# Performance work log

Hardware: AMD Instinct MI355X
Metric: run time of the kernel (lower is better)

Reference implementation:

```python
import jax, jax.numpy as jnp
import numpy as np

N = 100000      # nodes
E = 300000      # directed edges (avg degree ~3, ogbn-arxiv-like sparsity)
F_IN = 128      # ogbn-arxiv node features
H = 256         # hidden
C = 40          # ogbn-arxiv classes
L = 6           # num_layers
BN_EPS = 1e-5


def setup_inputs() -> dict:
    key = jax.random.key(0)
    ks = jax.random.split(key, 12)
    x = jax.random.normal(ks[0], (N, F_IN), jnp.float32)
    edge_index = jax.random.randint(ks[1], (2, E), 0, N, dtype=jnp.int32)
    s_in = 1.0 / np.sqrt(F_IN)
    s_h = 1.0 / np.sqrt(H)
    return {
        "x": x,
        "edge_index": edge_index,
        "w_in": jax.random.normal(ks[2], (F_IN, H), jnp.float32) * s_in,
        "b_in": jnp.zeros((H,), jnp.float32),
        "conv_w": jax.random.normal(ks[3], (L, H, H), jnp.float32) * s_h,
        "conv_b": jnp.zeros((L, H), jnp.float32),
        "bn_gamma": jnp.ones((L, H), jnp.float32),
        "bn_beta": jnp.zeros((L, H), jnp.float32),
        "out_w": jax.random.normal(ks[4], (H, C), jnp.float32) * s_h,
        "out_b": jnp.zeros((C,), jnp.float32),
        "res_weights": jax.random.normal(ks[5], (L,), jnp.float32),
    }


def _gcn_norm(edge_index, n_nodes):
    # GCNConv default: add self-loops, symmetric normalization D^-1/2 (A+I) D^-1/2
    loops = jnp.arange(n_nodes, dtype=edge_index.dtype)
    src = jnp.concatenate([edge_index[0], loops])
    dst = jnp.concatenate([edge_index[1], loops])
    deg = jax.ops.segment_sum(jnp.ones_like(dst, jnp.float32), dst, num_segments=n_nodes)
    dinv = jax.lax.rsqrt(jnp.maximum(deg, 1.0))
    norm = dinv[src] * dinv[dst]  # [E+N]
    return src, dst, norm


def _batchnorm(h, gamma, beta):
    # BatchNorm1d in training mode: biased batch statistics over nodes
    m = jnp.mean(h, axis=0)
    v = jnp.mean(jnp.square(h - m), axis=0)
    return (h - m) * jax.lax.rsqrt(v + BN_EPS) * gamma + beta


def reference(x, edge_index, w_in, b_in, conv_w, conv_b, bn_gamma, bn_beta, out_w, out_b, res_weights):
    src, dst, norm = _gcn_norm(edge_index, N)
    h = x @ w_in + b_in            # input_fc: [N, H]
    x_input = h
    layer_out = []
    prev = None
    for i in range(L):
        hw = h @ conv_w[i]                                  # linear transform
        msg = hw[src] * norm[:, None]                       # gather + scale
        agg = jax.ops.segment_sum(msg, dst, num_segments=N) + conv_b[i]  # scatter-add
        a = jax.nn.relu(_batchnorm(agg, bn_gamma[i], bn_beta[i]))
        # dropout p=0.5 omitted (eval mode / deterministic reference)
        if i == 0:
            h = a + 0.2 * x_input
        else:
            h = a + 0.2 * x_input + 0.7 * prev
        layer_out.append(h)
        prev = h
    w = jax.nn.softmax(res_weights)                          # [L]
    mix = jnp.einsum('lnh,l->nh', jnp.stack(layer_out), w)   # weighted sum of layer outputs
    logits = mix @ out_w + out_b                             # [N, C]
    return jax.nn.log_softmax(logits, axis=1)
```

## Files before the change

kernel.cpp:

```cpp
#include <hip/hip_runtime.h>
#include <math.h>

#define Nn   100000
#define Ee   300000
#define FIN  128
#define Hdim 256
#define Ncls 40
#define Lnum 6
#define SCAN_B 98
#define KP   264
#define EMAX 1152

typedef __attribute__((ext_vector_type(8))) short bf16x8;
typedef __attribute__((ext_vector_type(4))) float f32x4;

__device__ __forceinline__ float bf2f(unsigned int u16) {
    unsigned int x = u16 << 16;
    return __builtin_bit_cast(float, x);
}
__device__ __forceinline__ unsigned short f2bf(float f) {
    unsigned int x = __builtin_bit_cast(unsigned int, f);
    x = (x + 0x7FFFu + ((x >> 16) & 1u)) >> 16;
    return (unsigned short)x;
}
__device__ __forceinline__ void unpack2(unsigned int u, float& lo, float& hi) {
    lo = __builtin_bit_cast(float, u << 16);
    hi = __builtin_bit_cast(float, u & 0xFFFF0000u);
}
__device__ __forceinline__ unsigned int pack2(float a, float b) {
    return (unsigned int)f2bf(a) | ((unsigned int)f2bf(b) << 16);
}
__device__ __forceinline__ void acc8(float* a, float w, uint4 v) {
    float f0, f1;
    unpack2(v.x, f0, f1); a[0] += w * f0; a[1] += w * f1;
    unpack2(v.y, f0, f1); a[2] += w * f0; a[3] += w * f1;
    unpack2(v.z, f0, f1); a[4] += w * f0; a[5] += w * f1;
    unpack2(v.w, f0, f1); a[6] += w * f0; a[7] += w * f1;
}

__global__ void count_edges(const int* __restrict__ ei, int* __restrict__ cnt) {
    int e = blockIdx.x * blockDim.x + threadIdx.x;
    if (e < Ee) atomicAdd(&cnt[ei[Ee + e]], 1);
}

__global__ void scan_block(const int* __restrict__ cnt, int* __restrict__ iscan,
                           int* __restrict__ btot) {
    __shared__ int buf[1024];
    int t = threadIdx.x;
    int g = blockIdx.x * 1024 + t;
    int v = (g < Nn) ? cnt[g] : 0;
    buf[t] = v; __syncthreads();
    for (int off = 1; off < 1024; off <<= 1) {
        int x = buf[t];
        int a = (t >= off) ? buf[t - off] : 0;
        __syncthreads();
        buf[t] = x + a;
        __syncthreads();
    }
    if (g < Nn) iscan[g] = buf[t];
    if (t == 1023) btot[blockIdx.x] = buf[1023];
}

__global__ void scan_tops(const int* __restrict__ btot, int* __restrict__ bpref) {
    __shared__ int b[128];
    int t = threadIdx.x;
    int v = (t < SCAN_B) ? btot[t] : 0;
    b[t] = v; __syncthreads();
    for (int off = 1; off < 128; off <<= 1) {
        int x = b[t];
        int a = (t >= off) ? b[t - off] : 0;
        __syncthreads();
        b[t] = x + a;
        __syncthreads();
    }
    if (t < SCAN_B) bpref[t] = b[t] - v;
}

__global__ void scan_final(const int* __restrict__ cnt, const int* __restrict__ iscan,
                           const int* __restrict__ bpref, int* __restrict__ offs,
                           float* __restrict__ dinvp) {
    int g = blockIdx.x * 1024 + threadIdx.x;
    if (g < Nn) {
        int c = cnt[g];
        offs[g] = bpref[blockIdx.x] + iscan[g] - c;
        dinvp[g] = rsqrtf((float)(c + 1));
    }
    if (g == 0) offs[Nn] = Ee;
}

__global__ void fill_csr(const int* __restrict__ ei, const int* __restrict__ offs,
                         int* __restrict__ cur, const float* __restrict__ dinvp,
                         int* __restrict__ esrc, float* __restrict__ ew) {
    int e = blockIdx.x * blockDim.x + threadIdx.x;
    if (e >= Ee) return;
    int s = ei[e], d = ei[Ee + e];
    int p = offs[d] + atomicAdd(&cur[d], 1);
    esrc[p] = s;
    ew[p] = dinvp[s];
}

__global__ void prep_weights(const float* __restrict__ conv_w, const float* __restrict__ w_in,
                             const float* __restrict__ out_w,
                             unsigned short* __restrict__ Whi,
                             unsigned short* __restrict__ Fhi,
                             unsigned short* __restrict__ Whd, unsigned short* __restrict__ Wld) {
    int b = blockIdx.x, t = threadIdx.x;
    if (b < 1536) {
        int id = b * 256 + t;
        int l = id >> 16, k = (id >> 8) & 255, n = id & 255;
        Whi[l * 65536 + n * 256 + k] = f2bf(conv_w[id]);
    } else if (b < 1664) {
        int id = (b - 1536) * 256 + t;
        int k = id >> 8, n = id & 255;
        Fhi[n * FIN + k] = f2bf(w_in[id]);
    } else {
        int id = (b - 1664) * 256 + t;
        int c = id >> 8, k = id & 255;
        float w = (c < Ncls) ? out_w[k * Ncls + c] : 0.f;
        unsigned short hi = f2bf(w);
        unsigned short lo = f2bf(w - bf2f(hi));
        Whd[c * 256 + k] = hi;
        Wld[c * 256 + k] = lo;
    }
}

__global__ void cvt_bf16(const float* __restrict__ src, unsigned short* __restrict__ dst, int n8) {
    int i = blockIdx.x * blockDim.x + threadIdx.x;
    if (i >= n8) return;
    float4 a = ((const float4*)src)[i * 2];
    float4 b = ((const float4*)src)[i * 2 + 1];
    uint4 o;
    o.x = pack2(a.x, a.y); o.y = pack2(a.z, a.w);
    o.z = pack2(b.x, b.y); o.w = pack2(b.z, b.w);
    ((uint4*)dst)[i] = o;
}

__global__ void bn_reduce(const float* __restrict__ P, float* __restrict__ bnsum,
                          float* __restrict__ bnsq, int nb) {
    int c = threadIdx.x;
    int per = (nb + gridDim.x - 1) / gridDim.x;
    int r0 = blockIdx.x * per;
    int r1 = r0 + per; if (r1 > nb) r1 = nb;
    float s = 0.f, q = 0.f;
    for (int r = r0; r < r1; ++r) {
        s += P[(size_t)r * 512 + c];
        q += P[(size_t)r * 512 + 256 + c];
    }
    if (r0 < r1) {
        atomicAdd(&bnsum[c], s);
        atomicAdd(&bnsq[c], q);
    }
}

__global__ __launch_bounds__(512) void gemm_mfma(
    const unsigned short* __restrict__ A, unsigned short* __restrict__ C,
    const unsigned short* __restrict__ W,
    const float* __restrict__ bias, int K, int nrows)
{
    __shared__ __align__(16) unsigned short smem[18432];

    const int t    = threadIdx.x;
    const int lane = t & 63, wid = t >> 6;
    const int ln   = lane & 15, quad = lane >> 4;
    const int r64  = (wid >> 2) * 64, c64 = (wid & 3) * 64;
    const int r0   = blockIdx.x * 128;

    unsigned short* At = smem;
    unsigned short* Bt = smem + 5120;

    f32x4 acc[4][4];
#pragma unroll
    for (int i = 0; i < 4; ++i)
#pragma unroll
        for (int j = 0; j < 4; ++j) acc[i][j] = (f32x4){0.f, 0.f, 0.f, 0.f};

    const int arow = t >> 2, akq = t & 3;
    const bool arow_ok = (r0 + arow < nrows);
    const int nk = K >> 5;

    uint4 ga = make_uint4(0u, 0u, 0u, 0u);
    if (arow_ok) ga = *(const uint4*)&A[(size_t)(r0 + arow) * K + akq * 8];
    uint4 gb[2];
#pragma unroll
    for (int q = 0; q < 2; ++q) {
        int idx = t + 512 * q, row = idx >> 2, kq = idx & 3;
        gb[q] = *(const uint4*)&W[(size_t)row * K + kq * 8];
    }

    for (int kt = 0; kt < nk; ++kt) {
        __syncthreads();
        *(uint4*)&At[arow * 40 + akq * 8] = ga;
#pragma unroll
        for (int q = 0; q < 2; ++q) {
            int idx = t + 512 * q, row = idx >> 2, kq = idx & 3;
            *(uint4*)&Bt[row * 40 + kq * 8] = gb[q];
        }
        __syncthreads();
        if (kt + 1 < nk) {
            int k0 = (kt + 1) << 5;
            ga = make_uint4(0u, 0u, 0u, 0u);
            if (arow_ok) ga = *(const uint4*)&A[(size_t)(r0 + arow) * K + k0 + akq * 8];
#pragma unroll
            for (int q = 0; q < 2; ++q) {
                int idx = t + 512 * q, row = idx >> 2, kq = idx & 3;
                gb[q] = *(const uint4*)&W[(size_t)row * K + k0 + kq * 8];
            }
        }
        bf16x8 af[4], bf[4];
#pragma unroll
        for (int rt = 0; rt < 4; ++rt)
            af[rt] = *(const bf16x8*)&At[(r64 + rt * 16 + ln) * 40 + quad * 8];
#pragma unroll
        for (int ct = 0; ct < 4; ++ct)
            bf[ct] = *(const bf16x8*)&Bt[(c64 + ct * 16 + ln) * 40 + quad * 8];
#pragma unroll
        for (int rt = 0; rt < 4; ++rt)
#pragma unroll
            for (int ct = 0; ct < 4; ++ct)
                acc[rt][ct] = __builtin_amdgcn_mfma_f32_16x16x32_bf16(af[rt], bf[ct], acc[rt][ct], 0, 0, 0);
    }
    __syncthreads();

    float bc[4];
#pragma unroll
    for (int ct = 0; ct < 4; ++ct) bc[ct] = bias[c64 + ct * 16 + ln];

    unsigned short* Tt = &smem[wid * 2304];
    const int rr2 = lane & 31, jh = lane >> 5;
#pragma unroll
    for (int h = 0; h < 2; ++h) {
#pragma unroll
        for (int rr = 0; rr < 2; ++rr) {
            int rt = 2 * h + rr;
#pragma unroll
            for (int ct = 0; ct < 4; ++ct)
#pragma unroll
                for (int v = 0; v < 4; ++v)
                    Tt[(rr * 16 + quad * 4 + v) * 72 + ct * 16 + ln] = f2bf(acc[rt][ct][v] + bc[ct]);
        }
        __asm__ volatile("s_waitcnt lgkmcnt(0)" ::: "memory");
        int grow = r0 + r64 + h * 32 + rr2;
        if (grow < nrows) {
#pragma unroll
            for (int j = 0; j < 4; ++j) {
                uint4 v4 = *(const uint4*)&Tt[rr2 * 72 + jh * 32 + j * 8];
                *(uint4*)&C[(size_t)grow * 256 + c64 + jh * 32 + j * 8] = v4;
            }
        }
        __asm__ volatile("s_waitcnt lgkmcnt(0)" ::: "memory");
    }
}

__global__ __launch_bounds__(512, 4) void gemm_agg(
    const unsigned short* __restrict__ Hin,
    unsigned short* __restrict__ C,
    const unsigned short* __restrict__ W,
    const float* __restrict__ bias,
    const int* __restrict__ offs, const int* __restrict__ esrc,
    const float* __restrict__ ew, const float* __restrict__ dinvp,
    float* __restrict__ bnsum, float* __restrict__ bnsq,
    float* __restrict__ Pstats)
{
    __shared__ __align__(16) unsigned short At[128 * KP];
    __shared__ __align__(16) uint2 eL[EMAX];
    __shared__ int oL[132];
    __shared__ float lsum[256], lsq[256];

    const int t    = threadIdx.x;
    const int lane = t & 63, wid = t >> 6;
    const int ln   = lane & 15, quad = lane >> 4;
    const int r64  = (wid >> 2) * 64, c64 = (wid & 3) * 64;
    const int r0   = blockIdx.x * 128;

    if (t < 256) { lsum[t] = 0.f; lsq[t] = 0.f; }

    const int rEnd = (r0 + 128 <= Nn) ? (r0 + 128) : Nn;
    const int E0 = offs[r0];
    const int E1 = offs[rEnd];
    const int nE = E1 - E0;
    const bool staged = (nE <= EMAX);

    if (t < 129) {
        int idx = r0 + t; if (idx > Nn) idx = Nn;
        oL[t] = offs[idx];
    }
    if (staged) {
        for (int j = t; j < nE; j += 512)
            eL[j] = make_uint2((unsigned)esrc[E0 + j],
                               __builtin_bit_cast(unsigned, ew[E0 + j]));
    }
    __syncthreads();

    const int half = lane >> 5, l31 = lane & 31;
    const int base = wid * 16 + half * 8;
#pragma unroll 1
    for (int p = 0; p < 4; ++p) {
        const int rA = base + 2 * p, rB = rA + 1;
        const int nA = r0 + rA, nB = r0 + rB;
        float a[8] = {0.f,0.f,0.f,0.f,0.f,0.f,0.f,0.f};
        float b[8] = {0.f,0.f,0.f,0.f,0.f,0.f,0.f,0.f};
        int eA = oL[rA], eA1 = oL[rA + 1];
        int eB = oL[rB], eB1 = oL[rB + 1];
        float dnA = 0.f, dnB = 0.f;
        if (nA < Nn) {
            dnA = dinvp[nA];
            uint4 u = *(const uint4*)&Hin[(size_t)nA * Hdim + l31 * 8];
            acc8(a, dnA, u);
        }
        if (nB < Nn) {
            dnB = dinvp[nB];
            uint4 u = *(const uint4*)&Hin[(size_t)nB * Hdim + l31 * 8];
            acc8(b, dnB, u);
        }
        if (staged) {
            while (eA < eA1 || eB < eB1) {
                bool dA = eA < eA1, dB = eB < eB1;
                uint4 vA, vB; float wA = 0.f, wB = 0.f;
                if (dA) {
                    uint2 s = eL[eA - E0];
                    wA = __builtin_bit_cast(float, s.y);
                    vA = *(const uint4*)&Hin[(size_t)s.x * Hdim + l31 * 8];
                }
                if (dB) {
                    uint2 s = eL[eB - E0];
                    wB = __builtin_bit_cast(float, s.y);
                    vB = *(const uint4*)&Hin[(size_t)s.x * Hdim + l31 * 8];
                }
                if (dA) { acc8(a, wA, vA); ++eA; }
                if (dB) { acc8(b, wB, vB); ++eB; }
            }
        } else {
            for (int e = eA; e < eA1; ++e) {
                int s = esrc[e]; float w = ew[e];
                uint4 v = *(const uint4*)&Hin[(size_t)s * Hdim + l31 * 8];
                acc8(a, w, v);
            }
            for (int e = eB; e < eB1; ++e) {
                int s = esrc[e]; float w = ew[e];
                uint4 v = *(const uint4*)&Hin[(size_t)s * Hdim + l31 * 8];
                acc8(b, w, v);
            }
        }
#pragma unroll
        for (int k = 0; k < 8; ++k) { a[k] *= dnA; b[k] *= dnB; }
        *(uint4*)&At[rA * KP + l31 * 8] =
            make_uint4(pack2(a[0], a[1]), pack2(a[2], a[3]),
                       pack2(a[4], a[5]), pack2(a[6], a[7]));
        *(uint4*)&At[rB * KP + l31 * 8] =
            make_uint4(pack2(b[0], b[1]), pack2(b[2], b[3]),
                       pack2(b[4], b[5]), pack2(b[6], b[7]));
    }
    __syncthreads();

    f32x4 acc[4][4];
#pragma unroll
    for (int i = 0; i < 4; ++i)
#pragma unroll
        for (int j = 0; j < 4; ++j) acc[i][j] = (f32x4){0.f, 0.f, 0.f, 0.f};

#pragma unroll
    for (int kt = 0; kt < 8; ++kt) {
        bf16x8 af[4], bf[4];
#pragma unroll
        for (int ct = 0; ct < 4; ++ct)
            bf[ct] = *(const bf16x8*)&W[(size_t)(c64 + ct * 16 + ln) * 256 + kt * 32 + quad * 8];
#pragma unroll
        for (int rt = 0; rt < 4; ++rt)
            af[rt] = *(const bf16x8*)&At[(r64 + rt * 16 + ln) * KP + kt * 32 + quad * 8];
#pragma unroll
        for (int rt = 0; rt < 4; ++rt)
#pragma unroll
            for (int ct = 0; ct < 4; ++ct)
                acc[rt][ct] = __builtin_amdgcn_mfma_f32_16x16x32_bf16(af[rt], bf[ct], acc[rt][ct], 0, 0, 0);
    }

    float bc[4];
#pragma unroll
    for (int ct = 0; ct < 4; ++ct) bc[ct] = bias[c64 + ct * 16 + ln];

#pragma unroll
    for (int ct = 0; ct < 4; ++ct) {
        float s = 0.f, qq = 0.f;
#pragma unroll
        for (int rt = 0; rt < 4; ++rt)
#pragma unroll
            for (int v = 0; v < 4; ++v) {
                int row = r0 + r64 + rt * 16 + quad * 4 + v;
                if (row < Nn) {
                    float val = acc[rt][ct][v] + bc[ct];
                    s += val; qq += val * val;
                }
            }
        s  += __shfl_xor(s, 16);  s  += __shfl_xor(s, 32);
        qq += __shfl_xor(qq, 16); qq += __shfl_xor(qq, 32);
        if (quad == 0) { atomicAdd(&lsum[c64 + ct * 16 + ln], s); atomicAdd(&lsq[c64 + ct * 16 + ln], qq); }
    }

    __syncthreads();

#pragma unroll
    for (int rt = 0; rt < 4; ++rt)
#pragma unroll
        for (int ct = 0; ct < 4; ++ct)
#pragma unroll
            for (int v = 0; v < 4; ++v)
                At[(r64 + rt * 16 + quad * 4 + v) * KP + c64 + ct * 16 + ln] =
                    f2bf(acc[rt][ct][v] + bc[ct]);
    __syncthreads();

    const int l31s = t & 31, rhalf = t >> 5;
#pragma unroll
    for (int p = 0; p < 8; ++p) {
        int lrow = p * 16 + rhalf;
        int grow = r0 + lrow;
        if (grow < Nn) {
            uint4 v4 = *(const uint4*)&At[lrow * KP + l31s * 8];
            *(uint4*)&C[(size_t)grow * 256 + l31s * 8] = v4;
        }
    }

    if (t < 256) {
        if (Pstats) {
            Pstats[(size_t)blockIdx.x * 512 + t]       = lsum[t];
            Pstats[(size_t)blockIdx.x * 512 + 256 + t] = lsq[t];
        } else {
            atomicAdd(&bnsum[t], lsum[t]);
            atomicAdd(&bnsq[t], lsq[t]);
        }
    }
}

__global__ void apply_kernel(const unsigned short* __restrict__ T,
                             const unsigned short* __restrict__ X,
                             unsigned short* __restrict__ Hb, unsigned short* __restrict__ M,
                             const float* __restrict__ bnsum, const float* __restrict__ bnsq,
                             const float* __restrict__ gamma, const float* __restrict__ beta,
                             const float* __restrict__ res_w, int layer) {
    __shared__ float sc[256], sh[256];
    int t = threadIdx.x;
    {
        float mean = bnsum[t] * (1.0f / Nn);
        float var  = fmaxf(bnsq[t] * (1.0f / Nn) - mean * mean, 0.f);
        float rstd = rsqrtf(var + 1e-5f);
        float s = gamma[t] * rstd;
        sc[t] = s; sh[t] = beta[t] - mean * s;
    }
    float m0 = res_w[0];
#pragma unroll
    for (int i = 1; i < Lnum; ++i) m0 = fmaxf(m0, res_w[i]);
    float se = 0.f, wl = 0.f;
#pragma unroll
    for (int i = 0; i < Lnum; ++i) {
        float e = __expf(res_w[i] - m0);
        se += e;
        if (i == layer) wl = e;
    }
    float wi = wl / se;
    __syncthreads();

    int idx = blockIdx.x * blockDim.x + t;
    int c8 = idx & 31;
    float scl[8], shl[8];
#pragma unroll
    for (int k = 0; k < 8; ++k) { scl[k] = sc[c8 * 8 + k]; shl[k] = sh[c8 * 8 + k]; }

    uint4 tv = ((const uint4*)T)[idx];
    uint4 xv = ((const uint4*)X)[idx];
    float tf[8], xf[8];
    unpack2(tv.x, tf[0], tf[1]); unpack2(tv.y, tf[2], tf[3]);
    unpack2(tv.z, tf[4], tf[5]); unpack2(tv.w, tf[6], tf[7]);
    unpack2(xv.x, xf[0], xf[1]); unpack2(xv.y, xf[2], xf[3]);
    unpack2(xv.z, xf[4], xf[5]); unpack2(xv.w, xf[6], xf[7]);

    float a[8];
#pragma unroll
    for (int k = 0; k < 8; ++k)
        a[k] = fmaxf(tf[k] * scl[k] + shl[k], 0.f) + 0.2f * xf[k];
    if (layer > 0) {
        uint4 hv = ((const uint4*)Hb)[idx];
        float hf[8];
        unpack2(hv.x, hf[0], hf[1]); unpack2(hv.y, hf[2], hf[3]);
        unpack2(hv.z, hf[4], hf[5]); unpack2(hv.w, hf[6], hf[7]);
#pragma unroll
        for (int k = 0; k < 8; ++k) a[k] += 0.7f * hf[k];
    }
    uint4 ho;
    ho.x = pack2(a[0], a[1]); ho.y = pack2(a[2], a[3]);
    ho.z = pack2(a[4], a[5]); ho.w = pack2(a[6], a[7]);
    ((uint4*)Hb)[idx] = ho;

    float m[8];
    if (layer == 0) {
#pragma unroll
        for (int k = 0; k < 8; ++k) m[k] = wi * a[k];
    } else {
        uint4 mv = ((const uint4*)M)[idx];
        float mf[8];
        unpack2(mv.x, mf[0], mf[1]); unpack2(mv.y, mf[2], mf[3]);
        unpack2(mv.z, mf[4], mf[5]); unpack2(mv.w, mf[6], mf[7]);
#pragma unroll
        for (int k = 0; k < 8; ++k) m[k] = mf[k] + wi * a[k];
    }
    uint4 mo;
    mo.x = pack2(m[0], m[1]); mo.y = pack2(m[2], m[3]);
    mo.z = pack2(m[4], m[5]); mo.w = pack2(m[6], m[7]);
    ((uint4*)M)[idx] = mo;
}

__global__ __launch_bounds__(512) void head_mfma(const unsigned short* __restrict__ M,
                                                 const unsigned short* __restrict__ Whd,
                                                 const unsigned short* __restrict__ Wld,
                                                 const float* __restrict__ out_b,
                                                 float* __restrict__ out, int nrows) {
    __shared__ unsigned short At[128 * 40];
    const int t    = threadIdx.x;
    const int lane = t & 63, wid = t >> 6;
    const int ln   = lane & 15, quad = lane >> 4;
    const int r0   = blockIdx.x * 128;

    f32x4 acc[3];
#pragma unroll
    for (int ct = 0; ct < 3; ++ct) acc[ct] = (f32x4){0.f, 0.f, 0.f, 0.f};

    for (int k0 = 0; k0 < 256; k0 += 32) {
        __syncthreads();
        {
            int row = t >> 2, kq = t & 3;
            uint4 g = make_uint4(0u, 0u, 0u, 0u);
            if (r0 + row < nrows)
                g = *(const uint4*)&M[(size_t)(r0 + row) * 256 + k0 + kq * 8];
            *(uint4*)&At[row * 40 + kq * 8] = g;
        }
        __syncthreads();
        bf16x8 af = *(const bf16x8*)&At[(wid * 16 + ln) * 40 + quad * 8];
#pragma unroll
        for (int ct = 0; ct < 3; ++ct) {
            int c = ct * 16 + ln;
            bf16x8 bh = *(const bf16x8*)&Whd[c * 256 + k0 + quad * 8];
            bf16x8 bl = *(const bf16x8*)&Wld[c * 256 + k0 + quad * 8];
            acc[ct] = __builtin_amdgcn_mfma_f32_16x16x32_bf16(af, bh, acc[ct], 0, 0, 0);
            acc[ct] = __builtin_amdgcn_mfma_f32_16x16x32_bf16(af, bl, acc[ct], 0, 0, 0);
        }
    }

    int   cc[3]; float bias[3];
#pragma unroll
    for (int ct = 0; ct < 3; ++ct) {
        cc[ct] = ct * 16 + ln;
        bias[ct] = (cc[ct] < Ncls) ? out_b[cc[ct]] : 0.f;
    }
#pragma unroll
    for (int v = 0; v < 4; ++v) {
        int row = r0 + wid * 16 + quad * 4 + v;
        float val[3];
#pragma unroll
        for (int ct = 0; ct < 3; ++ct) val[ct] = acc[ct][v] + bias[ct];
        float mx = -1e30f;
#pragma unroll
        for (int ct = 0; ct < 3; ++ct) if (cc[ct] < Ncls) mx = fmaxf(mx, val[ct]);
        mx = fmaxf(mx, __shfl_xor(mx, 1)); mx = fmaxf(mx, __shfl_xor(mx, 2));
        mx = fmaxf(mx, __shfl_xor(mx, 4)); mx = fmaxf(mx, __shfl_xor(mx, 8));
        float s = 0.f;
#pragma unroll
        for (int ct = 0; ct < 3; ++ct) if (cc[ct] < Ncls) s += __expf(val[ct] - mx);
        s += __shfl_xor(s, 1); s += __shfl_xor(s, 2);
        s += __shfl_xor(s, 4); s += __shfl_xor(s, 8);
        float lse = mx + __logf(s);
        if (row < nrows) {
            out[(size_t)row * Ncls + cc[0]] = val[0] - lse;
            out[(size_t)row * Ncls + cc[1]] = val[1] - lse;
            if (ln < 8) out[(size_t)row * Ncls + cc[2]] = val[2] - lse;
        }
    }
}

extern "C" void kernel_launch(void* const* d_in, const int* in_sizes, int n_in,
                              void* d_out, int out_size, void* d_ws, size_t ws_size,
                              hipStream_t stream)
{
    const float* x      = (const float*)d_in[0];
    const int*   ei     = (const int*)d_in[1];
    const float* w_in   = (const float*)d_in[2];
    const float* b_in   = (const float*)d_in[3];
    const float* conv_w = (const float*)d_in[4];
    const float* conv_b = (const float*)d_in[5];
    const float* gamma  = (const float*)d_in[6];
    const float* beta   = (const float*)d_in[7];
    const float* out_w  = (const float*)d_in[8];
    const float* out_b  = (const float*)d_in[9];
    const float* res_w  = (const float*)d_in[10];
    float* out = (float*)d_out;
    char* ws = (char*)d_ws;

    int*   cnt    = (int*)  (ws + 0);
    int*   cursor = (int*)  (ws + 400000);
    int*   offs   = (int*)  (ws + 800000);
    float* dinvp  = (float*)(ws + 1200016);
    int*   esrc   = (int*)  (ws + 1600016);
    float* ew     = (float*)(ws + 2800016);
    int*   iscan  = (int*)  (ws + 4002064);
    int*   btot   = (int*)  (ws + 4402064);
    int*   bpref  = (int*)  (ws + 4402576);
    unsigned short* Whi = (unsigned short*)(ws + 4403088);
    unsigned short* Fhi = (unsigned short*)(ws + 5975952);
    unsigned short* Whd = (unsigned short*)(ws + 6107024);
    unsigned short* Wld = (unsigned short*)(ws + 6131600);
    unsigned short* X   = (unsigned short*)(ws + 6156176);
    unsigned short* Hb  = X  + (size_t)Nn * Hdim;
    unsigned short* T   = Hb + (size_t)Nn * Hdim;
    unsigned short* M   = T  + (size_t)Nn * Hdim;
    unsigned short* xbf = M;

    float* bnA = (float*)(ws + 4002064);

    const int gblocks = (Nn + 127) / 128;

    const size_t P_OFS = 6156176 + 4 * (size_t)Nn * Hdim * sizeof(unsigned short);
    const size_t P_BYTES = (size_t)gblocks * 512 * sizeof(float);
    float* Pst = (ws_size >= P_OFS + P_BYTES) ? (float*)(ws + P_OFS) : nullptr;

    hipMemsetAsync(cnt, 0, 800000, stream);

    count_edges<<<(Ee + 255) / 256, 256, 0, stream>>>(ei, cnt);
    scan_block<<<SCAN_B, 1024, 0, stream>>>(cnt, iscan, btot);
    scan_tops<<<1, 128, 0, stream>>>(btot, bpref);
    scan_final<<<SCAN_B, 1024, 0, stream>>>(cnt, iscan, bpref, offs, dinvp);
    fill_csr<<<(Ee + 255) / 256, 256, 0, stream>>>(ei, offs, cursor, dinvp, esrc, ew);

    hipMemsetAsync(bnA, 0, Lnum * 512 * sizeof(float), stream);

    prep_weights<<<1712, 256, 0, stream>>>(conv_w, w_in, out_w,
                                           Whi, Fhi, Whd, Wld);
    cvt_bf16<<<(Nn * FIN / 8 + 255) / 256, 256, 0, stream>>>(x, xbf, Nn * FIN / 8);

    gemm_mfma<<<gblocks, 512, 0, stream>>>(xbf, X, Fhi, b_in, FIN, Nn);

    for (int i = 0; i < Lnum; ++i) {
        float* bnsumL = bnA + (size_t)i * 512;
        float* bnsqL  = bnsumL + 256;
        gemm_agg<<<gblocks, 512, 0, stream>>>(i == 0 ? X : Hb, T,
                                              Whi + (size_t)i * Hdim * Hdim,
                                              conv_b + (size_t)i * Hdim,
                                              offs, esrc, ew, dinvp,
                                              bnsumL, bnsqL, Pst);
        if (Pst)
            bn_reduce<<<64, 256, 0, stream>>>(Pst, bnsumL, bnsqL, gblocks);
        apply_kernel<<<(Nn * 32) / 256, 256, 0, stream>>>(T, X, Hb, M,
                                                          bnsumL, bnsqL,
                                                          gamma + (size_t)i * Hdim,
                                                          beta + (size_t)i * Hdim,
                                                          res_w, i);
    }

    head_mfma<<<gblocks, 512, 0, stream>>>(M, Whd, Wld, out_b, out, Nn);
}
```

Before: 1.033 ms.

## Shrink gemm_agg tile to 64 rows and gather four rows per half-wave

Reduces the fused aggregate+GEMM block tile from 128 to 64 rows, which halves the LDS footprint and doubles the grid size so more blocks can be resident and the irregular gather work is spread more evenly. Each half-wave now aggregates four destination rows at once in a single loop, giving more independent gather loads in flight per iteration. The price is that each W fragment loaded per block feeds half as many MFMAs, so W traffic per output row doubles, and more per-block BN partial stats have to be reduced.

```diff
diff --git a/kernel.cpp b/kernel.cpp
--- a/kernel.cpp
+++ b/kernel.cpp
@@ -9,7 +9,7 @@
 #define Lnum 6
 #define SCAN_B 98
 #define KP   264
-#define EMAX 1152
+#define EMAX 768
 
 typedef __attribute__((ext_vector_type(8))) short bf16x8;
 typedef __attribute__((ext_vector_type(4))) float f32x4;
@@ -261,26 +261,26 @@
     float* __restrict__ bnsum, float* __restrict__ bnsq,
     float* __restrict__ Pstats)
 {
-    __shared__ __align__(16) unsigned short At[128 * KP];
+    __shared__ __align__(16) unsigned short At[64 * KP];
     __shared__ __align__(16) uint2 eL[EMAX];
-    __shared__ int oL[132];
+    __shared__ int oL[68];
     __shared__ float lsum[256], lsq[256];
 
     const int t    = threadIdx.x;
     const int lane = t & 63, wid = t >> 6;
     const int ln   = lane & 15, quad = lane >> 4;
-    const int r64  = (wid >> 2) * 64, c64 = (wid & 3) * 64;
-    const int r0   = blockIdx.x * 128;
+    const int wr32 = (wid >> 2) * 32, c64 = (wid & 3) * 64;
+    const int r0   = blockIdx.x * 64;
 
     if (t < 256) { lsum[t] = 0.f; lsq[t] = 0.f; }
 
-    const int rEnd = (r0 + 128 <= Nn) ? (r0 + 128) : Nn;
+    const int rEnd = (r0 + 64 <= Nn) ? (r0 + 64) : Nn;
     const int E0 = offs[r0];
     const int E1 = offs[rEnd];
     const int nE = E1 - E0;
     const bool staged = (nE <= EMAX);
 
-    if (t < 129) {
+    if (t < 65) {
         int idx = r0 + t; if (idx > Nn) idx = Nn;
         oL[t] = offs[idx];
     }
@@ -292,83 +292,88 @@
     __syncthreads();
 
     const int half = lane >> 5, l31 = lane & 31;
-    const int base = wid * 16 + half * 8;
-#pragma unroll 1
-    for (int p = 0; p < 4; ++p) {
-        const int rA = base + 2 * p, rB = rA + 1;
-        const int nA = r0 + rA, nB = r0 + rB;
-        float a[8] = {0.f,0.f,0.f,0.f,0.f,0.f,0.f,0.f};
-        float b[8] = {0.f,0.f,0.f,0.f,0.f,0.f,0.f,0.f};
-        int eA = oL[rA], eA1 = oL[rA + 1];
-        int eB = oL[rB], eB1 = oL[rB + 1];
-        float dnA = 0.f, dnB = 0.f;
-        if (nA < Nn) {
-            dnA = dinvp[nA];
-            uint4 u = *(const uint4*)&Hin[(size_t)nA * Hdim + l31 * 8];
-            acc8(a, dnA, u);
-        }
-        if (nB < Nn) {
-            dnB = dinvp[nB];
-            uint4 u = *(const uint4*)&Hin[(size_t)nB * Hdim + l31 * 8];
-            acc8(b, dnB, u);
-        }
+    const int rb = (wid * 2 + half) * 4;
+    {
+        float a0[8] = {0,0,0,0,0,0,0,0}, a1[8] = {0,0,0,0,0,0,0,0};
+        float a2[8] = {0,0,0,0,0,0,0,0}, a3[8] = {0,0,0,0,0,0,0,0};
+        const int n0 = r0 + rb, n1 = n0 + 1, n2 = n0 + 2, n3 = n0 + 3;
+        int e0 = oL[rb],     f0 = oL[rb + 1];
+        int e1 = oL[rb + 1], f1 = oL[rb + 2];
+        int e2 = oL[rb + 2], f2 = oL[rb + 3];
+        int e3 = oL[rb + 3], f3 = oL[rb + 4];
+        float dn0 = 0.f, dn1 = 0.f, dn2 = 0.f, dn3 = 0.f;
+        if (n0 < Nn) { dn0 = dinvp[n0];
+            acc8(a0, dn0, *(const uint4*)&Hin[(size_t)n0 * Hdim + l31 * 8]); }
+        if (n1 < Nn) { dn1 = dinvp[n1];
+            acc8(a1, dn1, *(const uint4*)&Hin[(size_t)n1 * Hdim + l31 * 8]); }
+        if (n2 < Nn) { dn2 = dinvp[n2];
+            acc8(a2, dn2, *(const uint4*)&Hin[(size_t)n2 * Hdim + l31 * 8]); }
+        if (n3 < Nn) { dn3 = dinvp[n3];
+            acc8(a3, dn3, *(const uint4*)&Hin[(size_t)n3 * Hdim + l31 * 8]); }
         if (staged) {
-            while (eA < eA1 || eB < eB1) {
-                bool dA = eA < eA1, dB = eB < eB1;
-                uint4 vA, vB; float wA = 0.f, wB = 0.f;
-                if (dA) {
-                    uint2 s = eL[eA - E0];
-                    wA = __builtin_bit_cast(float, s.y);
-                    vA = *(const uint4*)&Hin[(size_t)s.x * Hdim + l31 * 8];
-                }
-                if (dB) {
-                    uint2 s = eL[eB - E0];
-                    wB = __builtin_bit_cast(float, s.y);
-                    vB = *(const uint4*)&Hin[(size_t)s.x * Hdim + l31 * 8];
-                }
-                if (dA) { acc8(a, wA, vA); ++eA; }
-                if (dB) { acc8(b, wB, vB); ++eB; }
+            while ((e0 < f0) | (e1 < f1) | (e2 < f2) | (e3 < f3)) {
+                bool d0 = e0 < f0, d1 = e1 < f1, d2 = e2 < f2, d3 = e3 < f3;
+                uint4 v0 = make_uint4(0u,0u,0u,0u), v1 = v0, v2 = v0, v3 = v0;
+                float w0 = 0.f, w1 = 0.f, w2 = 0.f, w3 = 0.f;
+                if (d0) { uint2 s = eL[e0 - E0]; w0 = __builtin_bit_cast(float, s.y);
+                          v0 = *(const uint4*)&Hin[(size_t)s.x * Hdim + l31 * 8]; }
+                if (d1) { uint2 s = eL[e1 - E0]; w1 = __builtin_bit_cast(float, s.y);
+                          v1 = *(const uint4*)&Hin[(size_t)s.x * Hdim + l31 * 8]; }
+                if (d2) { uint2 s = eL[e2 - E0]; w2 = __builtin_bit_cast(float, s.y);
+                          v2 = *(const uint4*)&Hin[(size_t)s.x * Hdim + l31 * 8]; }
+                if (d3) { uint2 s = eL[e3 - E0]; w3 = __builtin_bit_cast(float, s.y);
+                          v3 = *(const uint4*)&Hin[(size_t)s.x * Hdim + l31 * 8]; }
+                if (d0) { acc8(a0, w0, v0); ++e0; }
+                if (d1) { acc8(a1, w1, v1); ++e1; }
+                if (d2) { acc8(a2, w2, v2); ++e2; }
+                if (d3) { acc8(a3, w3, v3); ++e3; }
             }
         } else {
-            for (int e = eA; e < eA1; ++e) {
-                int s = esrc[e]; float w = ew[e];
-                uint4 v = *(const uint4*)&Hin[(size_t)s * Hdim + l31 * 8];
-                acc8(a, w, v);
-            }
-            for (int e = eB; e < eB1; ++e) {
-                int s = esrc[e]; float w = ew[e];
-                uint4 v = *(const uint4*)&Hin[(size_t)s * Hdim + l31 * 8];
-                acc8(b, w, v);
-            }
-        }
-#pragma unroll
-        for (int k = 0; k < 8; ++k) { a[k] *= dnA; b[k] *= dnB; }
-        *(uint4*)&At[rA * KP + l31 * 8] =
-            make_uint4(pack2(a[0], a[1]), pack2(a[2], a[3]),
-                       pack2(a[4], a[5]), pack2(a[6], a[7]));
-        *(uint4*)&At[rB * KP + l31 * 8] =
-            make_uint4(pack2(b[0], b[1]), pack2(b[2], b[3]),
-                       pack2(b[4], b[5]), pack2(b[6], b[7]));
+            for (int e = e0; e < f0; ++e) {
+                acc8(a0, ew[e], *(const uint4*)&Hin[(size_t)esrc[e] * Hdim + l31 * 8]); }
+            for (int e = e1; e < f1; ++e) {
+                acc8(a1, ew[e], *(const uint4*)&Hin[(size_t)esrc[e] * Hdim + l31 * 8]); }
+            for (int e = e2; e < f2; ++e) {
+                acc8(a2, ew[e], *(const uint4*)&Hin[(size_t)esrc[e] * Hdim + l31 * 8]); }
+            for (int e = e3; e < f3; ++e) {
+                acc8(a3, ew[e], *(const uint4*)&Hin[(size_t)esrc[e] * Hdim + l31 * 8]); }
+        }
+#pragma unroll
+        for (int k = 0; k < 8; ++k) {
+            a0[k] *= dn0; a1[k] *= dn1; a2[k] *= dn2; a3[k] *= dn3;
+        }
+        *(uint4*)&At[(rb + 0) * KP + l31 * 8] =
+            make_uint4(pack2(a0[0], a0[1]), pack2(a0[2], a0[3]),
+                       pack2(a0[4], a0[5]), pack2(a0[6], a0[7]));
+        *(uint4*)&At[(rb + 1) * KP + l31 * 8] =
+            make_uint4(pack2(a1[0], a1[1]), pack2(a1[2], a1[3]),
+                       pack2(a1[4], a1[5]), pack2(a1[6], a1[7]));
+        *(uint4*)&At[(rb + 2) * KP + l31 * 8] =
+            make_uint4(pack2(a2[0], a2[1]), pack2(a2[2], a2[3]),
+                       pack2(a2[4], a2[5]), pack2(a2[6], a2[7]));
+        *(uint4*)&At[(rb + 3) * KP + l31 * 8] =
+            make_uint4(pack2(a3[0], a3[1]), pack2(a3[2], a3[3]),
+                       pack2(a3[4], a3[5]), pack2(a3[6], a3[7]));
     }
     __syncthreads();
 
-    f32x4 acc[4][4];
-#pragma unroll
-    for (int i = 0; i < 4; ++i)
+    f32x4 acc[2][4];
+#pragma unroll
+    for (int i = 0; i < 2; ++i)
 #pragma unroll
         for (int j = 0; j < 4; ++j) acc[i][j] = (f32x4){0.f, 0.f, 0.f, 0.f};
 
 #pragma unroll
     for (int kt = 0; kt < 8; ++kt) {
-        bf16x8 af[4], bf[4];
+        bf16x8 af[2], bf[4];
 #pragma unroll
         for (int ct = 0; ct < 4; ++ct)
             bf[ct] = *(const bf16x8*)&W[(size_t)(c64 + ct * 16 + ln) * 256 + kt * 32 + quad * 8];
 #pragma unroll
-        for (int rt = 0; rt < 4; ++rt)
-            af[rt] = *(const bf16x8*)&At[(r64 + rt * 16 + ln) * KP + kt * 32 + quad * 8];
-#pragma unroll
-        for (int rt = 0; rt < 4; ++rt)
+        for (int rt = 0; rt < 2; ++rt)
+            af[rt] = *(const bf16x8*)&At[(wr32 + rt * 16 + ln) * KP + kt * 32 + quad * 8];
+#pragma unroll
+        for (int rt = 0; rt < 2; ++rt)
 #pragma unroll
             for (int ct = 0; ct < 4; ++ct)
                 acc[rt][ct] = __builtin_amdgcn_mfma_f32_16x16x32_bf16(af[rt], bf[ct], acc[rt][ct], 0, 0, 0);
@@ -382,10 +387,10 @@
     for (int ct = 0; ct < 4; ++ct) {
         float s = 0.f, qq = 0.f;
 #pragma unroll
-        for (int rt = 0; rt < 4; ++rt)
+        for (int rt = 0; rt < 2; ++rt)
 #pragma unroll
             for (int v = 0; v < 4; ++v) {
-                int row = r0 + r64 + rt * 16 + quad * 4 + v;
+                int row = r0 + wr32 + rt * 16 + quad * 4 + v;
                 if (row < Nn) {
                     float val = acc[rt][ct][v] + bc[ct];
                     s += val; qq += val * val;
@@ -399,18 +404,18 @@
     __syncthreads();
 
 #pragma unroll
-    for (int rt = 0; rt < 4; ++rt)
+    for (int rt = 0; rt < 2; ++rt)
 #pragma unroll
         for (int ct = 0; ct < 4; ++ct)
 #pragma unroll
             for (int v = 0; v < 4; ++v)
-                At[(r64 + rt * 16 + quad * 4 + v) * KP + c64 + ct * 16 + ln] =
+                At[(wr32 + rt * 16 + quad * 4 + v) * KP + c64 + ct * 16 + ln] =
                     f2bf(acc[rt][ct][v] + bc[ct]);
     __syncthreads();
 
     const int l31s = t & 31, rhalf = t >> 5;
 #pragma unroll
-    for (int p = 0; p < 8; ++p) {
+    for (int p = 0; p < 4; ++p) {
         int lrow = p * 16 + rhalf;
         int grow = r0 + lrow;
         if (grow < Nn) {
@@ -614,9 +619,10 @@
     float* bnA = (float*)(ws + 4002064);
 
     const int gblocks = (Nn + 127) / 128;
+    const int ablocks = (Nn + 63) / 64;
 
     const size_t P_OFS = 6156176 + 4 * (size_t)Nn * Hdim * sizeof(unsigned short);
-    const size_t P_BYTES = (size_t)gblocks * 512 * sizeof(float);
+    const size_t P_BYTES = (size_t)ablocks * 512 * sizeof(float);
     float* Pst = (ws_size >= P_OFS + P_BYTES) ? (float*)(ws + P_OFS) : nullptr;
 
     hipMemsetAsync(cnt, 0, 800000, stream);
@@ -638,13 +644,13 @@
     for (int i = 0; i < Lnum; ++i) {
         float* bnsumL = bnA + (size_t)i * 512;
         float* bnsqL  = bnsumL + 256;
-        gemm_agg<<<gblocks, 512, 0, stream>>>(i == 0 ? X : Hb, T,
+        gemm_agg<<<ablocks, 512, 0, stream>>>(i == 0 ? X : Hb, T,
                                               Whi + (size_t)i * Hdim * Hdim,
                                               conv_b + (size_t)i * Hdim,
                                               offs, esrc, ew, dinvp,
                                               bnsumL, bnsqL, Pst);
         if (Pst)
-            bn_reduce<<<64, 256, 0, stream>>>(Pst, bnsumL, bnsqL, gblocks);
+            bn_reduce<<<64, 256, 0, stream>>>(Pst, bnsumL, bnsqL, ablocks);
         apply_kernel<<<(Nn * 32) / 256, 256, 0, stream>>>(T, X, Hb, M,
                                                           bnsumL, bnsqL,
                                                           gamma + (size_t)i * Hdim,
```

Result: slower. 1.157 ms (+12.0%).
